# Kernel optimization log

Measured on AMD Instinct MI355X. Metric: run time of the kernel, lower is better.

The kernel has to match this reference:

```python
import jax, jax.numpy as jnp
import numpy as np

NUM_NODES = 262144
NUM_VARS = NUM_NODES // 4
HIDDEN = 256
NUM_PROPS = 8
NUM_GRAPHS = 512


def setup_inputs() -> dict:
    key = jax.random.key(0)
    ks = jax.random.split(key, 12)
    node_embeddings = jax.random.normal(ks[0], (NUM_NODES, HIDDEN), dtype=jnp.float32)
    batch = jnp.sort(jax.random.randint(ks[1], (NUM_NODES,), 0, NUM_GRAPHS, dtype=jnp.int32))
    var_property_probs = jax.random.uniform(ks[2], (NUM_VARS, NUM_PROPS), dtype=jnp.float32)
    # every 4th node is a variable (node_type 0) -> exactly NUM_VARS variable nodes
    node_types = (jnp.arange(NUM_NODES, dtype=jnp.int32) % 4).astype(jnp.int32)
    s = 1.0 / np.sqrt(HIDDEN)
    sp = 1.0 / np.sqrt(NUM_PROPS)
    sq = 1.0 / np.sqrt(HIDDEN // 4)
    s2 = 1.0 / np.sqrt(2 * HIDDEN)
    params = {
        'W_pre': jax.random.uniform(ks[3], (HIDDEN, HIDDEN), jnp.float32, -s, s),
        'b_pre': jax.random.uniform(ks[4], (HIDDEN,), jnp.float32, -s, s),
        'W1': jax.random.uniform(ks[5], (NUM_PROPS, HIDDEN // 4), jnp.float32, -sp, sp),
        'b1': jax.random.uniform(ks[6], (HIDDEN // 4,), jnp.float32, -sp, sp),
        'W2': jax.random.uniform(ks[7], (HIDDEN // 4, 1), jnp.float32, -sq, sq),
        'b2': jax.random.uniform(ks[8], (1,), jnp.float32, -sq, sq),
        'W_post': jax.random.uniform(ks[9], (2 * HIDDEN, HIDDEN), jnp.float32, -s2, s2),
        'b_post': jax.random.uniform(ks[10], (HIDDEN,), jnp.float32, -s2, s2),
    }
    return dict(node_embeddings=node_embeddings, batch=batch,
                var_property_probs=var_property_probs, node_types=node_types, **params)


def reference(node_embeddings, batch, var_property_probs, node_types,
              W_pre, b_pre, W1, b1, W2, b2, W_post, b_post):
    # pre-readout linear: [N, H]
    h = node_embeddings @ W_pre + b_pre

    # gating MLP over variable properties -> per-variable weight in (0,1)
    gate = jax.nn.sigmoid(jax.nn.relu(var_property_probs @ W1 + b1) @ W2 + b2)  # [num_vars, 1]

    # scatter gate values onto variable nodes (node_types == 0), weight 1 elsewhere
    var_mask = node_types == 0                                    # [N]
    var_idx = jnp.cumsum(var_mask.astype(jnp.int32)) - 1          # k-th var node -> row k of gate
    var_idx = jnp.clip(var_idx, 0, gate.shape[0] - 1)
    node_w = jnp.where(var_mask[:, None], gate[var_idx], 1.0)     # [N, 1]
    h = h * node_w

    # segment mean
    sums = jax.ops.segment_sum(h, batch, num_segments=NUM_GRAPHS, indices_are_sorted=True)
    counts = jax.ops.segment_sum(jnp.ones((h.shape[0],), h.dtype), batch,
                                 num_segments=NUM_GRAPHS, indices_are_sorted=True)
    h_mean = sums / jnp.maximum(counts, 1.0)[:, None]

    # segment max (empty segments -> 0, matching torch_scatter fill)
    h_max = jax.ops.segment_max(h, batch, num_segments=NUM_GRAPHS, indices_are_sorted=True)
    h_max = jnp.where(jnp.isfinite(h_max), h_max, 0.0)

    h_combined = jnp.concatenate([h_mean, h_max], axis=-1)        # [B, 2H]
    return h_combined @ W_post + b_post                            # [B, H]
```

## Files before the change

kernel.cpp:

```cpp
#include <hip/hip_runtime.h>

#define N_NODES 262144
#define N_VARS  65536
#define HID     256
#define NGRAPH  512

#define OFF_WBT   0u
#define OFF_GATE  131072u
#define OFF_NODEW 393216u
#define OFF_GSUM  1441792u
#define OFF_GMAX  1966080u
#define OFF_GCNT  2490368u
#define OFF_CCNT  2492416u
#define OFF_COFF  2493440u

typedef float f32x4 __attribute__((ext_vector_type(4)));
typedef short s16x8 __attribute__((ext_vector_type(8)));

__device__ __forceinline__ unsigned short f2bf(float f) {
    unsigned u = __float_as_uint(f);
    unsigned r = u + 0x7fffu + ((u >> 16) & 1u);
    return (unsigned short)(r >> 16);
}

__device__ __forceinline__ unsigned fmax_key(float f) {
    unsigned u = __float_as_uint(f);
    return (u & 0x80000000u) ? ~u : (u | 0x80000000u);
}

__global__ void k_pack(const float* __restrict__ W, unsigned short* __restrict__ wbt) {
    int n = blockIdx.x, k = threadIdx.x;
    wbt[n * 256 + k] = f2bf(W[k * 256 + n]);
}

__global__ void k_gate(const float* __restrict__ vpp, const float* __restrict__ W1,
                       const float* __restrict__ b1, const float* __restrict__ W2,
                       const float* __restrict__ b2, float* __restrict__ gate) {
    __shared__ float sW1[512], sb1[64], sW2[64], sb2;
    int t = threadIdx.x;
    sW1[t] = W1[t];
    sW1[t + 256] = W1[t + 256];
    if (t < 64) { sb1[t] = b1[t]; sW2[t] = W2[t]; }
    if (t == 0) sb2 = b2[0];
    __syncthreads();
    int v = blockIdx.x * 256 + t;
    float4 p0 = ((const float4*)vpp)[v * 2];
    float4 p1 = ((const float4*)vpp)[v * 2 + 1];
    float p[8] = {p0.x, p0.y, p0.z, p0.w, p1.x, p1.y, p1.z, p1.w};
    float acc = sb2;
#pragma unroll 8
    for (int j = 0; j < 64; ++j) {
        float h = sb1[j];
#pragma unroll
        for (int q = 0; q < 8; ++q) h += p[q] * sW1[q * 64 + j];
        h = fmaxf(h, 0.f);
        acc += h * sW2[j];
    }
    gate[v] = 1.f / (1.f + expf(-acc));
}

__global__ void k_ccnt(const int* __restrict__ nt, unsigned* __restrict__ ccnt) {
    __shared__ unsigned s[256];
    int t = threadIdx.x;
    int4 v = ((const int4*)nt)[blockIdx.x * 256 + t];
    unsigned c = (unsigned)(v.x == 0) + (v.y == 0) + (v.z == 0) + (v.w == 0);
    s[t] = c;
    __syncthreads();
    for (int off = 128; off; off >>= 1) {
        if (t < off) s[t] += s[t + off];
        __syncthreads();
    }
    if (t == 0) ccnt[blockIdx.x] = s[0];
}

__global__ void k_scan(const unsigned* __restrict__ ccnt, unsigned* __restrict__ coff) {
    __shared__ unsigned s[256];
    int t = threadIdx.x;
    unsigned own = ccnt[t];
    s[t] = own;
    __syncthreads();
    for (int off = 1; off < 256; off <<= 1) {
        unsigned v = (t >= off) ? s[t - off] : 0u;
        __syncthreads();
        s[t] += v;
        __syncthreads();
    }
    coff[t] = s[t] - own;
}

__global__ void k_nodew(const int* __restrict__ nt, const unsigned* __restrict__ coff,
                        const float* __restrict__ gate, float* __restrict__ nodew) {
    __shared__ unsigned s[256];
    int t = threadIdx.x;
    int4 v = ((const int4*)nt)[blockIdx.x * 256 + t];
    unsigned m0 = (v.x == 0), m1 = (v.y == 0), m2 = (v.z == 0), m3 = (v.w == 0);
    unsigned c = m0 + m1 + m2 + m3;
    s[t] = c;
    __syncthreads();
    for (int off = 1; off < 256; off <<= 1) {
        unsigned u = (t >= off) ? s[t - off] : 0u;
        __syncthreads();
        s[t] += u;
        __syncthreads();
    }
    unsigned rank = coff[blockIdx.x] + s[t] - c;
    const unsigned cap = N_VARS - 1;
    float4 w;
    w.x = m0 ? gate[rank < cap ? rank : cap] : 1.f; rank += m0;
    w.y = m1 ? gate[rank < cap ? rank : cap] : 1.f; rank += m1;
    w.z = m2 ? gate[rank < cap ? rank : cap] : 1.f; rank += m2;
    w.w = m3 ? gate[rank < cap ? rank : cap] : 1.f;
    ((float4*)nodew)[blockIdx.x * 256 + t] = w;
}

__global__ void k_gcnt(const int* __restrict__ batch, unsigned* __restrict__ gcnt) {
    int g = threadIdx.x;
    int lo = 0, hi = N_NODES;
    while (lo < hi) { int mid = (lo + hi) >> 1; if (batch[mid] < g) lo = mid + 1; else hi = mid; }
    int lb0 = lo;
    lo = lb0; hi = N_NODES;
    while (lo < hi) { int mid = (lo + hi) >> 1; if (batch[mid] < g + 1) lo = mid + 1; else hi = mid; }
    gcnt[g] = (unsigned)(lo - lb0);
}

__global__ __launch_bounds__(256, 3) void k_main(
        const float* __restrict__ X, const int* __restrict__ batch,
        const float* __restrict__ nodew, const unsigned short* __restrict__ wbt,
        const float* __restrict__ bpre, float* __restrict__ gsum,
        unsigned* __restrict__ gmax) {
    __shared__ __align__(16) unsigned char smem[34432];
    float* hlds  = (float*)smem;
    float* sbpre = (float*)(smem + 32896);
    float* snw   = (float*)(smem + 33920);
    int*   sbt   = (int*)(smem + 34176);

    int t = threadIdx.x;
    int rowbase = blockIdx.x * 64;
    sbpre[t] = bpre[t];
    if (t < 64) { snw[t] = nodew[rowbase + t]; sbt[t] = batch[rowbase + t]; }

#pragma unroll
    for (int i = 0; i < 16; ++i) {
        int idx = t + 256 * i;
        int r = idx >> 6, cg = idx & 63;
        float4 v = ((const float4*)X)[(rowbase + r) * 64 + cg];
        unsigned lo = (unsigned)f2bf(v.x) | ((unsigned)f2bf(v.y) << 16);
        unsigned hi = (unsigned)f2bf(v.z) | ((unsigned)f2bf(v.w) << 16);
        int byte = (r * 512 + cg * 8) ^ ((r & 7) << 4);
        *(uint2*)(smem + byte) = make_uint2(lo, hi);
    }
    __syncthreads();

    int wave = t >> 6, lane = t & 63;
    int colbase = wave * 64;
    f32x4 acc[4][4];
#pragma unroll
    for (int r = 0; r < 4; ++r)
#pragma unroll
        for (int c = 0; c < 4; ++c)
#pragma unroll
            for (int q = 0; q < 4; ++q) acc[r][c][q] = 0.f;

    const unsigned short* wp[4];
#pragma unroll
    for (int c = 0; c < 4; ++c)
        wp[c] = wbt + (colbase + c * 16 + (lane & 15)) * 256 + ((lane >> 4) * 8);

#pragma unroll
    for (int kk = 0; kk < 8; ++kk) {
        s16x8 a[4], b[4];
#pragma unroll
        for (int r = 0; r < 4; ++r) {
            int row = r * 16 + (lane & 15);
            int byte = (row * 512 + (kk * 32 + (lane >> 4) * 8) * 2) ^ ((row & 7) << 4);
            a[r] = *(const s16x8*)(smem + byte);
        }
#pragma unroll
        for (int c = 0; c < 4; ++c) b[c] = *(const s16x8*)(wp[c] + kk * 32);
#pragma unroll
        for (int r = 0; r < 4; ++r)
#pragma unroll
            for (int c = 0; c < 4; ++c)
                asm volatile("v_mfma_f32_16x16x32_bf16 %0, %1, %2, %0"
                             : "+v"(acc[r][c]) : "v"(a[r]), "v"(b[c]));
    }
    asm volatile("s_nop 7\n\ts_nop 7\n\ts_nop 7" ::);
    __syncthreads();

    float sum = 0.f, mx = -3.4e38f;
    int g = sbt[0];
    auto flush = [&]() {
        atomicAdd(&gsum[g * 256 + t], sum);
        atomicMax(&gmax[g * 256 + t], fmax_key(mx));
    };

#pragma unroll
    for (int ph = 0; ph < 2; ++ph) {
#pragma unroll
        for (int r = 2 * ph; r < 2 * ph + 2; ++r) {
            int row0 = r * 16 + (lane >> 4) * 4;
#pragma unroll
            for (int c = 0; c < 4; ++c) {
                int col = colbase + c * 16 + (lane & 15);
                float bp = sbpre[col];
#pragma unroll
                for (int j = 0; j < 4; ++j) {
                    float vv = (acc[r][c][j] + bp) * snw[row0 + j];
                    hlds[(row0 + j - ph * 32) * 257 + col] = vv;
                }
            }
        }
        __syncthreads();
        for (int r = 0; r < 32; ++r) {
            int gg = sbt[ph * 32 + r];
            if (gg != g) { flush(); sum = 0.f; mx = -3.4e38f; g = gg; }
            float vv = hlds[r * 257 + t];
            sum += vv;
            mx = fmaxf(mx, vv);
        }
        __syncthreads();
    }
    flush();
}

__global__ void k_final(const float* __restrict__ gsum, const unsigned* __restrict__ gmax,
                        const unsigned* __restrict__ gcnt, const float* __restrict__ Wp,
                        const float* __restrict__ bp, float* __restrict__ out) {
    __shared__ float hrow[512];
    int g = blockIdx.x, j = threadIdx.x;
    unsigned cnt = gcnt[g];
    float inv = 1.f / (float)(cnt > 0u ? cnt : 1u);
    hrow[j] = gsum[g * 256 + j] * inv;
    unsigned key = gmax[g * 256 + j];
    float m = 0.f;
    if (cnt != 0u) {
        unsigned u = (key & 0x80000000u) ? (key ^ 0x80000000u) : ~key;
        m = __uint_as_float(u);
    }
    hrow[256 + j] = m;
    __syncthreads();
    float accv = bp[j];
#pragma unroll 8
    for (int k = 0; k < 512; ++k) accv += hrow[k] * Wp[k * 256 + j];
    out[g * 256 + j] = accv;
}

extern "C" void kernel_launch(void* const* d_in, const int* in_sizes, int n_in,
                              void* d_out, int out_size, void* d_ws, size_t ws_size,
                              hipStream_t stream) {
    const float* X      = (const float*)d_in[0];
    const int*   batch  = (const int*)d_in[1];
    const float* vpp    = (const float*)d_in[2];
    const int*   nt     = (const int*)d_in[3];
    const float* W_pre  = (const float*)d_in[4];
    const float* b_pre  = (const float*)d_in[5];
    const float* W1     = (const float*)d_in[6];
    const float* b1     = (const float*)d_in[7];
    const float* W2     = (const float*)d_in[8];
    const float* b2     = (const float*)d_in[9];
    const float* W_post = (const float*)d_in[10];
    const float* b_post = (const float*)d_in[11];
    float* out = (float*)d_out;

    char* ws = (char*)d_ws;
    unsigned short* wbt = (unsigned short*)(ws + OFF_WBT);
    float* gate  = (float*)(ws + OFF_GATE);
    float* nodew = (float*)(ws + OFF_NODEW);
    float* gsum  = (float*)(ws + OFF_GSUM);
    unsigned* gmax = (unsigned*)(ws + OFF_GMAX);
    unsigned* gcnt = (unsigned*)(ws + OFF_GCNT);
    unsigned* ccnt = (unsigned*)(ws + OFF_CCNT);
    unsigned* coff = (unsigned*)(ws + OFF_COFF);

    hipMemsetAsync(ws + OFF_GSUM, 0, 524288u * 2, stream);

    k_pack<<<256, 256, 0, stream>>>(W_pre, wbt);
    k_gate<<<256, 256, 0, stream>>>(vpp, W1, b1, W2, b2, gate);
    k_ccnt<<<256, 256, 0, stream>>>(nt, ccnt);
    k_scan<<<1, 256, 0, stream>>>(ccnt, coff);
    k_nodew<<<256, 256, 0, stream>>>(nt, coff, gate, nodew);
    k_gcnt<<<1, 512, 0, stream>>>(batch, gcnt);
    k_main<<<N_NODES / 64, 256, 0, stream>>>(X, batch, nodew, wbt, b_pre, gsum, gmax);
    k_final<<<NGRAPH, 256, 0, stream>>>(gsum, gmax, gcnt, W_post, b_post, out);
}
```

Measured before the change: 493.3 us.

## Assign one block per graph, fuse segment reduce and post-linear, merge prologue kernels

The main kernel now runs one block per graph. Each block walks its contiguous node range in 64-row tiles and keeps a register prefetch of the next X tile. Segment sum and max stay in registers and the W_post linear is fused at the end, which removes the global atomics, the memset, the k_final launch and several small prologue launches (pack, gate, ccnt and graph-start search are merged into one kernel). The cost is that only 512 blocks run, which on a large GPU means lower occupancy, and graphs of uneven size cause load imbalance.

Result: faster. 468.2 us (-5.1%).

```diff
diff --git a/kernel.cpp b/kernel.cpp
--- a/kernel.cpp
+++ b/kernel.cpp
@@ -8,14 +8,14 @@
 #define OFF_WBT   0u
 #define OFF_GATE  131072u
 #define OFF_NODEW 393216u
-#define OFF_GSUM  1441792u
-#define OFF_GMAX  1966080u
-#define OFF_GCNT  2490368u
-#define OFF_CCNT  2492416u
-#define OFF_COFF  2493440u
+#define OFF_GST   1441792u
+#define OFF_CCNT  1444352u
+#define OFF_COFF  1445376u
 
 typedef float f32x4 __attribute__((ext_vector_type(4)));
 typedef short s16x8 __attribute__((ext_vector_type(8)));
+
+#define BAR() asm volatile("s_waitcnt lgkmcnt(0)\n\ts_barrier" ::: "memory")
 
 __device__ __forceinline__ unsigned short f2bf(float f) {
     unsigned u = __float_as_uint(f);
@@ -23,54 +23,61 @@
     return (unsigned short)(r >> 16);
 }
 
-__device__ __forceinline__ unsigned fmax_key(float f) {
-    unsigned u = __float_as_uint(f);
-    return (u & 0x80000000u) ? ~u : (u | 0x80000000u);
-}
-
-__global__ void k_pack(const float* __restrict__ W, unsigned short* __restrict__ wbt) {
-    int n = blockIdx.x, k = threadIdx.x;
-    wbt[n * 256 + k] = f2bf(W[k * 256 + n]);
-}
-
-__global__ void k_gate(const float* __restrict__ vpp, const float* __restrict__ W1,
-                       const float* __restrict__ b1, const float* __restrict__ W2,
-                       const float* __restrict__ b2, float* __restrict__ gate) {
-    __shared__ float sW1[512], sb1[64], sW2[64], sb2;
-    int t = threadIdx.x;
-    sW1[t] = W1[t];
-    sW1[t + 256] = W1[t + 256];
-    if (t < 64) { sb1[t] = b1[t]; sW2[t] = W2[t]; }
-    if (t == 0) sb2 = b2[0];
-    __syncthreads();
-    int v = blockIdx.x * 256 + t;
-    float4 p0 = ((const float4*)vpp)[v * 2];
-    float4 p1 = ((const float4*)vpp)[v * 2 + 1];
-    float p[8] = {p0.x, p0.y, p0.z, p0.w, p1.x, p1.y, p1.z, p1.w};
-    float acc = sb2;
+__global__ void k_pre(const float* __restrict__ W, const float* __restrict__ vpp,
+                      const float* __restrict__ W1, const float* __restrict__ b1,
+                      const float* __restrict__ W2, const float* __restrict__ b2,
+                      const int* __restrict__ nt, const int* __restrict__ batch,
+                      unsigned short* __restrict__ wbt, float* __restrict__ gate,
+                      unsigned* __restrict__ ccnt, unsigned* __restrict__ gst) {
+    __shared__ float sm[664];
+    int b = blockIdx.x, t = threadIdx.x;
+
+    if (b < 256) {
+        wbt[b * 256 + t] = f2bf(W[t * 256 + b]);
+        return;
+    }
+    if (b < 512) {
+        float* sW1 = sm; float* sb1 = sm + 512; float* sW2 = sm + 576; float* sb2 = sm + 640;
+        sW1[t] = W1[t];
+        sW1[t + 256] = W1[t + 256];
+        if (t < 64) { sb1[t] = b1[t]; sW2[t] = W2[t]; }
+        if (t == 0) sb2[0] = b2[0];
+        __syncthreads();
+        int v = (b - 256) * 256 + t;
+        float4 p0 = ((const float4*)vpp)[v * 2];
+        float4 p1 = ((const float4*)vpp)[v * 2 + 1];
+        float p[8] = {p0.x, p0.y, p0.z, p0.w, p1.x, p1.y, p1.z, p1.w};
+        float acc = sb2[0];
 #pragma unroll 8
-    for (int j = 0; j < 64; ++j) {
-        float h = sb1[j];
-#pragma unroll
-        for (int q = 0; q < 8; ++q) h += p[q] * sW1[q * 64 + j];
-        h = fmaxf(h, 0.f);
-        acc += h * sW2[j];
-    }
-    gate[v] = 1.f / (1.f + expf(-acc));
-}
-
-__global__ void k_ccnt(const int* __restrict__ nt, unsigned* __restrict__ ccnt) {
-    __shared__ unsigned s[256];
-    int t = threadIdx.x;
-    int4 v = ((const int4*)nt)[blockIdx.x * 256 + t];
-    unsigned c = (unsigned)(v.x == 0) + (v.y == 0) + (v.z == 0) + (v.w == 0);
-    s[t] = c;
-    __syncthreads();
-    for (int off = 128; off; off >>= 1) {
-        if (t < off) s[t] += s[t + off];
-        __syncthreads();
-    }
-    if (t == 0) ccnt[blockIdx.x] = s[0];
+        for (int j = 0; j < 64; ++j) {
+            float h = sb1[j];
+#pragma unroll
+            for (int q = 0; q < 8; ++q) h += p[q] * sW1[q * 64 + j];
+            h = fmaxf(h, 0.f);
+            acc += h * sW2[j];
+        }
+        gate[v] = 1.f / (1.f + expf(-acc));
+        return;
+    }
+    if (b < 768) {
+        unsigned* s = (unsigned*)sm;
+        int chunk = b - 512;
+        int4 v = ((const int4*)nt)[chunk * 256 + t];
+        unsigned c = (unsigned)(v.x == 0) + (v.y == 0) + (v.z == 0) + (v.w == 0);
+        s[t] = c;
+        __syncthreads();
+        for (int off = 128; off; off >>= 1) {
+            if (t < off) s[t] += s[t + off];
+            __syncthreads();
+        }
+        if (t == 0) ccnt[chunk] = s[0];
+        return;
+    }
+    int g = (b - 768) * 256 + t;
+    int lo = 0, hi = N_NODES;
+    while (lo < hi) { int mid = (lo + hi) >> 1; if (batch[mid] < g) lo = mid + 1; else hi = mid; }
+    gst[g] = (unsigned)lo;
+    if (g == 0) gst[NGRAPH] = N_NODES;
 }
 
 __global__ void k_scan(const unsigned* __restrict__ ccnt, unsigned* __restrict__ coff) {
@@ -113,136 +120,132 @@
     ((float4*)nodew)[blockIdx.x * 256 + t] = w;
 }
 
-__global__ void k_gcnt(const int* __restrict__ batch, unsigned* __restrict__ gcnt) {
-    int g = threadIdx.x;
-    int lo = 0, hi = N_NODES;
-    while (lo < hi) { int mid = (lo + hi) >> 1; if (batch[mid] < g) lo = mid + 1; else hi = mid; }
-    int lb0 = lo;
-    lo = lb0; hi = N_NODES;
-    while (lo < hi) { int mid = (lo + hi) >> 1; if (batch[mid] < g + 1) lo = mid + 1; else hi = mid; }
-    gcnt[g] = (unsigned)(lo - lb0);
-}
-
-__global__ __launch_bounds__(256, 3) void k_main(
-        const float* __restrict__ X, const int* __restrict__ batch,
-        const float* __restrict__ nodew, const unsigned short* __restrict__ wbt,
-        const float* __restrict__ bpre, float* __restrict__ gsum,
-        unsigned* __restrict__ gmax) {
-    __shared__ __align__(16) unsigned char smem[34432];
+__global__ __launch_bounds__(256, 2) void k_main2(
+        const float* __restrict__ X, const float* __restrict__ nodew,
+        const unsigned short* __restrict__ wbt, const float* __restrict__ bpre,
+        const unsigned* __restrict__ gst, const float* __restrict__ Wpost,
+        const float* __restrict__ bpost, float* __restrict__ out) {
+    __shared__ __align__(16) unsigned char smem[36224];
     float* hlds  = (float*)smem;
     float* sbpre = (float*)(smem + 32896);
     float* snw   = (float*)(smem + 33920);
-    int*   sbt   = (int*)(smem + 34176);
+    float* hcomb = (float*)(smem + 34176);
 
     int t = threadIdx.x;
-    int rowbase = blockIdx.x * 64;
+    int g = blockIdx.x;
+    int rs = (int)gst[g], re = (int)gst[g + 1];
     sbpre[t] = bpre[t];
-    if (t < 64) { snw[t] = nodew[rowbase + t]; sbt[t] = batch[rowbase + t]; }
-
+
+    int wave = t >> 6, lane = t & 63;
+    int colbase = wave * 64;
+    const unsigned short* wp[4];
+#pragma unroll
+    for (int c = 0; c < 4; ++c)
+        wp[c] = wbt + (colbase + c * 16 + (lane & 15)) * 256 + ((lane >> 4) * 8);
+
+    float sumc = 0.f, maxc = -3.4e38f;
+
+    float4 pre[16];
 #pragma unroll
     for (int i = 0; i < 16; ++i) {
         int idx = t + 256 * i;
         int r = idx >> 6, cg = idx & 63;
-        float4 v = ((const float4*)X)[(rowbase + r) * 64 + cg];
-        unsigned lo = (unsigned)f2bf(v.x) | ((unsigned)f2bf(v.y) << 16);
-        unsigned hi = (unsigned)f2bf(v.z) | ((unsigned)f2bf(v.w) << 16);
-        int byte = (r * 512 + cg * 8) ^ ((r & 7) << 4);
-        *(uint2*)(smem + byte) = make_uint2(lo, hi);
-    }
-    __syncthreads();
-
-    int wave = t >> 6, lane = t & 63;
-    int colbase = wave * 64;
-    f32x4 acc[4][4];
-#pragma unroll
-    for (int r = 0; r < 4; ++r)
-#pragma unroll
-        for (int c = 0; c < 4; ++c)
-#pragma unroll
-            for (int q = 0; q < 4; ++q) acc[r][c][q] = 0.f;
-
-    const unsigned short* wp[4];
-#pragma unroll
-    for (int c = 0; c < 4; ++c)
-        wp[c] = wbt + (colbase + c * 16 + (lane & 15)) * 256 + ((lane >> 4) * 8);
-
-#pragma unroll
-    for (int kk = 0; kk < 8; ++kk) {
-        s16x8 a[4], b[4];
-#pragma unroll
-        for (int r = 0; r < 4; ++r) {
-            int row = r * 16 + (lane & 15);
-            int byte = (row * 512 + (kk * 32 + (lane >> 4) * 8) * 2) ^ ((row & 7) << 4);
-            a[r] = *(const s16x8*)(smem + byte);
-        }
-#pragma unroll
-        for (int c = 0; c < 4; ++c) b[c] = *(const s16x8*)(wp[c] + kk * 32);
+        int row = rs + r;
+        pre[i] = (row < re) ? ((const float4*)X)[row * 64 + cg] : make_float4(0.f, 0.f, 0.f, 0.f);
+    }
+
+    for (int tb = rs; tb < re; tb += 64) {
+#pragma unroll
+        for (int i = 0; i < 16; ++i) {
+            int idx = t + 256 * i;
+            int r = idx >> 6, cg = idx & 63;
+            unsigned lo = (unsigned)f2bf(pre[i].x) | ((unsigned)f2bf(pre[i].y) << 16);
+            unsigned hi = (unsigned)f2bf(pre[i].z) | ((unsigned)f2bf(pre[i].w) << 16);
+            int byte = (r * 512 + cg * 8) ^ ((r & 7) << 4);
+            *(uint2*)(smem + byte) = make_uint2(lo, hi);
+        }
+        if (t < 64) snw[t] = (tb + t < re) ? nodew[tb + t] : 0.f;
+        BAR();
+
+        if (tb + 64 < re) {
+#pragma unroll
+            for (int i = 0; i < 16; ++i) {
+                int idx = t + 256 * i;
+                int r = idx >> 6, cg = idx & 63;
+                int row = tb + 64 + r;
+                pre[i] = (row < re) ? ((const float4*)X)[row * 64 + cg]
+                                    : make_float4(0.f, 0.f, 0.f, 0.f);
+            }
+        }
+
+        f32x4 acc[4][4];
 #pragma unroll
         for (int r = 0; r < 4; ++r)
 #pragma unroll
             for (int c = 0; c < 4; ++c)
-                asm volatile("v_mfma_f32_16x16x32_bf16 %0, %1, %2, %0"
-                             : "+v"(acc[r][c]) : "v"(a[r]), "v"(b[c]));
-    }
-    asm volatile("s_nop 7\n\ts_nop 7\n\ts_nop 7" ::);
-    __syncthreads();
-
-    float sum = 0.f, mx = -3.4e38f;
-    int g = sbt[0];
-    auto flush = [&]() {
-        atomicAdd(&gsum[g * 256 + t], sum);
-        atomicMax(&gmax[g * 256 + t], fmax_key(mx));
-    };
-
-#pragma unroll
-    for (int ph = 0; ph < 2; ++ph) {
-#pragma unroll
-        for (int r = 2 * ph; r < 2 * ph + 2; ++r) {
-            int row0 = r * 16 + (lane >> 4) * 4;
-#pragma unroll
-            for (int c = 0; c < 4; ++c) {
-                int col = colbase + c * 16 + (lane & 15);
-                float bp = sbpre[col];
-#pragma unroll
-                for (int j = 0; j < 4; ++j) {
-                    float vv = (acc[r][c][j] + bp) * snw[row0 + j];
-                    hlds[(row0 + j - ph * 32) * 257 + col] = vv;
+#pragma unroll
+                for (int q = 0; q < 4; ++q) acc[r][c][q] = 0.f;
+
+#pragma unroll
+        for (int kk = 0; kk < 8; ++kk) {
+            s16x8 a[4], b[4];
+#pragma unroll
+            for (int r = 0; r < 4; ++r) {
+                int row = r * 16 + (lane & 15);
+                int byte = (row * 512 + (kk * 32 + (lane >> 4) * 8) * 2) ^ ((row & 7) << 4);
+                a[r] = *(const s16x8*)(smem + byte);
+            }
+#pragma unroll
+            for (int c = 0; c < 4; ++c) b[c] = *(const s16x8*)(wp[c] + kk * 32);
+#pragma unroll
+            for (int r = 0; r < 4; ++r)
+#pragma unroll
+                for (int c = 0; c < 4; ++c)
+                    asm volatile("v_mfma_f32_16x16x32_bf16 %0, %1, %2, %0"
+                                 : "+v"(acc[r][c]) : "v"(a[r]), "v"(b[c]));
+        }
+        asm volatile("s_nop 7\n\ts_nop 7\n\ts_nop 7" ::);
+        BAR();
+
+        int rem = re - tb; if (rem > 64) rem = 64;
+#pragma unroll
+        for (int ph = 0; ph < 2; ++ph) {
+#pragma unroll
+            for (int r = 2 * ph; r < 2 * ph + 2; ++r) {
+                int row0 = r * 16 + (lane >> 4) * 4;
+#pragma unroll
+                for (int c = 0; c < 4; ++c) {
+                    int col = colbase + c * 16 + (lane & 15);
+                    float bp = sbpre[col];
+#pragma unroll
+                    for (int j = 0; j < 4; ++j) {
+                        float vv = (acc[r][c][j] + bp) * snw[row0 + j];
+                        hlds[(row0 + j - ph * 32) * 257 + col] = vv;
+                    }
                 }
             }
-        }
-        __syncthreads();
-        for (int r = 0; r < 32; ++r) {
-            int gg = sbt[ph * 32 + r];
-            if (gg != g) { flush(); sum = 0.f; mx = -3.4e38f; g = gg; }
-            float vv = hlds[r * 257 + t];
-            sum += vv;
-            mx = fmaxf(mx, vv);
-        }
-        __syncthreads();
-    }
-    flush();
-}
-
-__global__ void k_final(const float* __restrict__ gsum, const unsigned* __restrict__ gmax,
-                        const unsigned* __restrict__ gcnt, const float* __restrict__ Wp,
-                        const float* __restrict__ bp, float* __restrict__ out) {
-    __shared__ float hrow[512];
-    int g = blockIdx.x, j = threadIdx.x;
-    unsigned cnt = gcnt[g];
-    float inv = 1.f / (float)(cnt > 0u ? cnt : 1u);
-    hrow[j] = gsum[g * 256 + j] * inv;
-    unsigned key = gmax[g * 256 + j];
-    float m = 0.f;
-    if (cnt != 0u) {
-        unsigned u = (key & 0x80000000u) ? (key ^ 0x80000000u) : ~key;
-        m = __uint_as_float(u);
-    }
-    hrow[256 + j] = m;
-    __syncthreads();
-    float accv = bp[j];
+            BAR();
+            int rlim = rem - ph * 32;
+            if (rlim > 32) rlim = 32;
+            for (int r = 0; r < rlim; ++r) {
+                float vv = hlds[r * 257 + t];
+                sumc += vv;
+                maxc = fmaxf(maxc, vv);
+            }
+            BAR();
+        }
+    }
+
+    int count = re - rs;
+    float mean = (count > 0) ? sumc / (float)count : 0.f;
+    float mx   = (count > 0) ? maxc : 0.f;
+    hcomb[t] = mean;
+    hcomb[256 + t] = mx;
+    BAR();
+    float accv = bpost[t];
 #pragma unroll 8
-    for (int k = 0; k < 512; ++k) accv += hrow[k] * Wp[k * 256 + j];
-    out[g * 256 + j] = accv;
+    for (int k = 0; k < 512; ++k) accv += hcomb[k] * Wpost[k * 256 + t];
+    out[g * 256 + t] = accv;
 }
 
 extern "C" void kernel_launch(void* const* d_in, const int* in_sizes, int n_in,
@@ -266,20 +269,13 @@
     unsigned short* wbt = (unsigned short*)(ws + OFF_WBT);
     float* gate  = (float*)(ws + OFF_GATE);
     float* nodew = (float*)(ws + OFF_NODEW);
-    float* gsum  = (float*)(ws + OFF_GSUM);
-    unsigned* gmax = (unsigned*)(ws + OFF_GMAX);
-    unsigned* gcnt = (unsigned*)(ws + OFF_GCNT);
+    unsigned* gst  = (unsigned*)(ws + OFF_GST);
     unsigned* ccnt = (unsigned*)(ws + OFF_CCNT);
     unsigned* coff = (unsigned*)(ws + OFF_COFF);
 
-    hipMemsetAsync(ws + OFF_GSUM, 0, 524288u * 2, stream);
-
-    k_pack<<<256, 256, 0, stream>>>(W_pre, wbt);
-    k_gate<<<256, 256, 0, stream>>>(vpp, W1, b1, W2, b2, gate);
-    k_ccnt<<<256, 256, 0, stream>>>(nt, ccnt);
+    k_pre<<<770, 256, 0, stream>>>(W_pre, vpp, W1, b1, W2, b2, nt, batch,
+                                   wbt, gate, ccnt, gst);
     k_scan<<<1, 256, 0, stream>>>(ccnt, coff);
     k_nodew<<<256, 256, 0, stream>>>(nt, coff, gate, nodew);
-    k_gcnt<<<1, 512, 0, stream>>>(batch, gcnt);
-    k_main<<<N_NODES / 64, 256, 0, stream>>>(X, batch, nodew, wbt, b_pre, gsum, gmax);
-    k_final<<<NGRAPH, 256, 0, stream>>>(gsum, gmax, gcnt, W_post, b_post, out);
-}
+    k_main2<<<NGRAPH, 256, 0, stream>>>(X, nodew, wbt, b_pre, gst, W_post, b_post, out);
+}
```
